# Optimization experiments

Hardware: AMD Instinct MI355X
Metric: run time of the kernel (lower is better)

The kernel has to match this reference:

```python
import jax, jax.numpy as jnp
import numpy as np

H = 8          # n_channels
NEIGHBORS = 5


def setup_inputs() -> dict:
    key = jax.random.key(0)
    k1, k2 = jax.random.split(key)
    B, N, C = 8, 1024, 256
    x = jax.random.normal(k1, (B, N, C), dtype=jnp.float32)
    # torch Linear weight: [out_features, in_features] = [2*H*C, C]
    W_qk = jax.random.normal(k2, (2 * H * C, C), dtype=jnp.float32) * (C ** -0.5)
    return {"x": x, "W_qk": W_qk}


def _forward(x, W_qk):
    B, N, C = x.shape
    scale = C ** -0.5
    qk = (x @ W_qk.T).reshape(B, N, 2, H, C).transpose(2, 0, 3, 1, 4)
    q, k = qk[0], qk[1]                              # [B,H,N,C]
    attn = jax.nn.softmax(jnp.einsum('bhnc,bhmc->bhnm', q, k) * scale, axis=-1)

    # clip(): top-k on detached channel-summed attention
    sum_edge = jnp.sum(jax.lax.stop_gradient(attn), axis=1)   # [B,N,N]
    _, index = jax.lax.top_k(sum_edge, NEIGHBORS)             # [B,N,NEIGHBORS]
    # Faithful to source: every mask row gets 1 at the union of ALL rows'
    # top-k indices (inner loop iterates over all rows of `inds`), plus eye(N).
    flat_idx = index.reshape(B, N * NEIGHBORS)                # [B, N*nb]
    col_mask = jnp.zeros((B, N), dtype=attn.dtype).at[
        jnp.arange(B)[:, None], flat_idx].set(1.0)            # [B,N]
    mask = jnp.maximum(jnp.eye(N, dtype=attn.dtype)[None], col_mask[:, None, :])  # [B,N,N]

    new_edge = mask[:, None] * attn                           # [B,H,N,N]

    # norm_edge(): row norm, then col norm, then row @ col^T
    norm_row = new_edge / (jnp.sum(new_edge, axis=-1, keepdims=True) + 1e-16)
    norm_col = norm_row / (jnp.sum(norm_row, axis=-2, keepdims=True) + 1e-16)
    return jnp.einsum('bhnm,bhkm->bhnk', norm_row, norm_col)  # [B,H,N,N]


def reference(x, W_qk):
    return _forward(x, W_qk)
```

## Files before the change

### kernel.cpp

```cpp
#include <hip/hip_runtime.h>
#include <hip/hip_bf16.h>
#include <cstdint>
#include <cstddef>

#define BB 8
#define HH 8
#define NN 1024
#define CC 256
#define OUTCH 4096

typedef __attribute__((ext_vector_type(8))) __bf16 bf16x8;
typedef __attribute__((ext_vector_type(4))) __bf16 bf16x4;
typedef __attribute__((ext_vector_type(4))) float f32x4;

__device__ inline void async16(const void* g, void* l)
{
  __builtin_amdgcn_global_load_lds(
      reinterpret_cast<const __attribute__((address_space(1))) unsigned int*>(
          reinterpret_cast<uintptr_t>(g)),
      reinterpret_cast<__attribute__((address_space(3))) unsigned int*>(
          reinterpret_cast<uintptr_t>(l)),
      16, 0, 0);
}

__device__ inline float waveMax(float v) {
#pragma unroll
  for (int o = 32; o > 0; o >>= 1) v = fmaxf(v, __shfl_xor(v, o, 64));
  return v;
}
__device__ inline float waveSum(float v) {
#pragma unroll
  for (int o = 32; o > 0; o >>= 1) v += __shfl_xor(v, o, 64);
  return v;
}

__global__ __launch_bounds__(256) void split2_kernel(
    const float* __restrict__ x, const float* __restrict__ W,
    __bf16* __restrict__ xh, __bf16* __restrict__ xl,
    __bf16* __restrict__ Wh, __bf16* __restrict__ Wl)
{
  const int NX = BB * NN * CC / 4;
  int i = blockIdx.x * 256 + threadIdx.x;
  const float* in; __bf16* ph; __bf16* pl; int j;
  if (i < NX) { in = x; ph = xh; pl = xl; j = i; }
  else        { in = W; ph = Wh; pl = Wl; j = i - NX; }
  const float4 v = ((const float4*)in)[j];
  bf16x4 h, l;
  h.x = (__bf16)v.x; l.x = (__bf16)(v.x - (float)h.x);
  h.y = (__bf16)v.y; l.y = (__bf16)(v.y - (float)h.y);
  h.z = (__bf16)v.z; l.z = (__bf16)(v.z - (float)h.z);
  h.w = (__bf16)v.w; l.w = (__bf16)(v.w - (float)h.w);
  ((bf16x4*)ph)[j] = h;
  ((bf16x4*)pl)[j] = l;
}

__global__ __launch_bounds__(256) void xw_mfma_kernel(
    const __bf16* __restrict__ Ah, const __bf16* __restrict__ Al,
    const __bf16* __restrict__ Bh, const __bf16* __restrict__ Bl,
    __bf16* __restrict__ Chi, __bf16* __restrict__ Clo)
{
  __shared__ __bf16 AsH[128 * 32], AsL[128 * 32], BsH[128 * 32], BsL[128 * 32];

  const int tid = threadIdx.x, lane = tid & 63, wid = tid >> 6;
  const int wr = wid >> 1, wc = wid & 1;
  const int bM = blockIdx.y * 128, bN = blockIdx.x * 128;

  const int srow = wid * 16 + (lane >> 2);
  const int scol = (lane & 3) * 8;
  const __bf16* gAh = Ah + (size_t)(bM + srow) * CC + scol;
  const __bf16* gAl = Al + (size_t)(bM + srow) * CC + scol;
  const __bf16* gBh = Bh + (size_t)(bN + srow) * CC + scol;
  const __bf16* gBl = Bl + (size_t)(bN + srow) * CC + scol;
  char* lAh = (char*)AsH + wid * 16 * 64;
  char* lAl = (char*)AsL + wid * 16 * 64;
  char* lBh = (char*)BsH + wid * 16 * 64;
  char* lBl = (char*)BsL + wid * 16 * 64;

  f32x4 acc[4][4];
  const f32x4 z = {0.f, 0.f, 0.f, 0.f};
#pragma unroll
  for (int m = 0; m < 4; ++m)
#pragma unroll
    for (int n = 0; n < 4; ++n) acc[m][n] = z;

  for (int k0 = 0; k0 < CC; k0 += 32) {
    async16(gAh + k0, lAh); async16(gAh + k0 + 64 * CC, lAh + 64 * 64);
    async16(gAl + k0, lAl); async16(gAl + k0 + 64 * CC, lAl + 64 * 64);
    async16(gBh + k0, lBh); async16(gBh + k0 + 64 * CC, lBh + 64 * 64);
    async16(gBl + k0, lBl); async16(gBl + k0 + 64 * CC, lBl + 64 * 64);
    __syncthreads();

    bf16x8 ah[4], al[4], bh_[4], bl_[4];
    const int fb = (lane & 15) * 64 + (lane >> 4) * 16;
#pragma unroll
    for (int m = 0; m < 4; ++m) {
      ah[m] = *(const bf16x8*)((const char*)AsH + (wr * 64 + m * 16) * 64 + fb);
      al[m] = *(const bf16x8*)((const char*)AsL + (wr * 64 + m * 16) * 64 + fb);
    }
#pragma unroll
    for (int n = 0; n < 4; ++n) {
      bh_[n] = *(const bf16x8*)((const char*)BsH + (wc * 64 + n * 16) * 64 + fb);
      bl_[n] = *(const bf16x8*)((const char*)BsL + (wc * 64 + n * 16) * 64 + fb);
    }
#pragma unroll
    for (int m = 0; m < 4; ++m)
#pragma unroll
      for (int n = 0; n < 4; ++n) {
        acc[m][n] = __builtin_amdgcn_mfma_f32_16x16x32_bf16(al[m], bh_[n], acc[m][n], 0, 0, 0);
        acc[m][n] = __builtin_amdgcn_mfma_f32_16x16x32_bf16(ah[m], bl_[n], acc[m][n], 0, 0, 0);
        acc[m][n] = __builtin_amdgcn_mfma_f32_16x16x32_bf16(ah[m], bh_[n], acc[m][n], 0, 0, 0);
      }
    __syncthreads();
  }

  const int fr = lane & 15;
  const int fq = lane >> 4;
#pragma unroll
  for (int m = 0; m < 4; ++m) {
    const int row0 = bM + wr * 64 + m * 16 + fq * 4;
#pragma unroll
    for (int n = 0; n < 4; ++n) {
      const int col = bN + wc * 64 + n * 16 + fr;
#pragma unroll
      for (int r = 0; r < 4; ++r) {
        const float v = acc[m][n][r];
        const __bf16 h = (__bf16)v;
        const __bf16 l = (__bf16)(v - (float)h);
        Chi[(size_t)(row0 + r) * OUTCH + col] = h;
        Clo[(size_t)(row0 + r) * OUTCH + col] = l;
      }
    }
  }
}

__global__ __launch_bounds__(256) void qkt_mfma_kernel(
    const __bf16* __restrict__ Qh, const __bf16* __restrict__ Ql,
    float* __restrict__ outall)
{
  const int f = blockIdx.x;
  const int xcd = f & 7;
  const int g = f >> 3;
  const int bh = xcd + 8 * (g >> 6);
  const int tile = g & 63;
  const int b = bh >> 3, h = bh & 7;
  const size_t qoff = (size_t)b * NN * OUTCH + (size_t)h * CC;
  const size_t koff = qoff + 2048;
  float* C = outall + ((size_t)bh << 20);

  __shared__ __bf16 AsH[128 * 32], AsL[128 * 32], BsH[128 * 32], BsL[128 * 32];

  const int tid = threadIdx.x, lane = tid & 63, wid = tid >> 6;
  const int wr = wid >> 1, wc = wid & 1;
  const int bM = (tile >> 3) * 128, bN = (tile & 7) * 128;

  const int srow = wid * 16 + (lane >> 2);
  const int scol = (lane & 3) * 8;
  const __bf16* gAh = Qh + qoff + (size_t)(bM + srow) * OUTCH + scol;
  const __bf16* gAl = Ql + qoff + (size_t)(bM + srow) * OUTCH + scol;
  const __bf16* gBh = Qh + koff + (size_t)(bN + srow) * OUTCH + scol;
  const __bf16* gBl = Ql + koff + (size_t)(bN + srow) * OUTCH + scol;
  char* lAh = (char*)AsH + wid * 16 * 64;
  char* lAl = (char*)AsL + wid * 16 * 64;
  char* lBh = (char*)BsH + wid * 16 * 64;
  char* lBl = (char*)BsL + wid * 16 * 64;

  f32x4 acc[4][4];
  const f32x4 z = {0.f, 0.f, 0.f, 0.f};
#pragma unroll
  for (int m = 0; m < 4; ++m)
#pragma unroll
    for (int n = 0; n < 4; ++n) acc[m][n] = z;

  for (int k0 = 0; k0 < CC; k0 += 32) {
    async16(gAh + k0, lAh); async16(gAh + k0 + (size_t)64 * OUTCH, lAh + 64 * 64);
    async16(gAl + k0, lAl); async16(gAl + k0 + (size_t)64 * OUTCH, lAl + 64 * 64);
    async16(gBh + k0, lBh); async16(gBh + k0 + (size_t)64 * OUTCH, lBh + 64 * 64);
    async16(gBl + k0, lBl); async16(gBl + k0 + (size_t)64 * OUTCH, lBl + 64 * 64);
    __syncthreads();

    bf16x8 ah[4], al[4], bh_[4], bl_[4];
    const int fb = (lane & 15) * 64 + (lane >> 4) * 16;
#pragma unroll
    for (int m = 0; m < 4; ++m) {
      ah[m] = *(const bf16x8*)((const char*)AsH + (wr * 64 + m * 16) * 64 + fb);
      al[m] = *(const bf16x8*)((const char*)AsL + (wr * 64 + m * 16) * 64 + fb);
    }
#pragma unroll
    for (int n = 0; n < 4; ++n) {
      bh_[n] = *(const bf16x8*)((const char*)BsH + (wc * 64 + n * 16) * 64 + fb);
      bl_[n] = *(const bf16x8*)((const char*)BsL + (wc * 64 + n * 16) * 64 + fb);
    }
#pragma unroll
    for (int m = 0; m < 4; ++m)
#pragma unroll
      for (int n = 0; n < 4; ++n) {
        acc[m][n] = __builtin_amdgcn_mfma_f32_16x16x32_bf16(al[m], bh_[n], acc[m][n], 0, 0, 0);
        acc[m][n] = __builtin_amdgcn_mfma_f32_16x16x32_bf16(ah[m], bl_[n], acc[m][n], 0, 0, 0);
        acc[m][n] = __builtin_amdgcn_mfma_f32_16x16x32_bf16(ah[m], bh_[n], acc[m][n], 0, 0, 0);
      }
    __syncthreads();
  }

  const int fr = lane & 15;
  const int fq = lane >> 4;
#pragma unroll
  for (int m = 0; m < 4; ++m) {
    const int row0 = bM + wr * 64 + m * 16 + fq * 4;
#pragma unroll
    for (int n = 0; n < 4; ++n) {
      const int col = bN + wc * 64 + n * 16 + fr;
#pragma unroll
      for (int r = 0; r < 4; ++r)
        C[(size_t)(row0 + r) * NN + col] = acc[m][n][r] * 0.0625f;
    }
  }
}

__global__ __launch_bounds__(256) void softmax_se_kernel(const float* __restrict__ logits,
                                                         __bf16* __restrict__ attnb,
                                                         float* __restrict__ se)
{
  const int bn = blockIdx.x;
  const int b = bn >> 10;
  const int n = bn & 1023;
  const int t = threadIdx.x;
  const int lane = t & 63, wv = t >> 6;
  __shared__ float wred[4];
  float4 acc = make_float4(0.f, 0.f, 0.f, 0.f);

#pragma unroll 1
  for (int h = 0; h < HH; ++h) {
    const size_t rowbase = (((size_t)(b * HH + h) << 10) + n) << 10;
    const float* ar = logits + rowbase;
    __bf16* arb = attnb + rowbase;
    float4 x = *(const float4*)(ar + (t << 2));
    float mx = waveMax(fmaxf(fmaxf(x.x, x.y), fmaxf(x.z, x.w)));
    if (lane == 0) wred[wv] = mx;
    __syncthreads();
    const float M = fmaxf(fmaxf(wred[0], wred[1]), fmaxf(wred[2], wred[3]));
    __syncthreads();

    float e0 = expf(x.x - M), e1 = expf(x.y - M), e2 = expf(x.z - M), e3 = expf(x.w - M);
    float s = waveSum(e0 + e1 + e2 + e3);
    if (lane == 0) wred[wv] = s;
    __syncthreads();
    const float inv = 1.0f / (wred[0] + wred[1] + wred[2] + wred[3]);

    const float o0 = e0 * inv, o1 = e1 * inv, o2 = e2 * inv, o3 = e3 * inv;
    bf16x4 ob; ob.x = (__bf16)o0; ob.y = (__bf16)o1; ob.z = (__bf16)o2; ob.w = (__bf16)o3;
    *(bf16x4*)(arb + (t << 2)) = ob;
    acc.x += o0; acc.y += o1; acc.z += o2; acc.w += o3;
    __syncthreads();
  }
  *(float4*)(se + (size_t)bn * NN + (t << 2)) = acc;
}

__global__ __launch_bounds__(256) void topk_kernel(const float* __restrict__ se,
                                                   float* __restrict__ colmask)
{
  const int bn = blockIdx.x;
  const int b = bn >> 10;
  const int t = threadIdx.x;
  __shared__ float vals[NN];
  __shared__ unsigned long long red[256];
  const float* rowp = se + (size_t)bn * NN;
  for (int i = t; i < NN; i += 256) vals[i] = rowp[i];
  __syncthreads();

  for (int it = 0; it < 5; ++it) {
    unsigned long long best = 0ull;
    for (int i = t; i < NN; i += 256) {
      const float v = vals[i];
      if (v >= 0.f) {
        unsigned long long key =
            ((unsigned long long)__float_as_uint(v) << 32) | (unsigned)(NN - 1 - i);
        if (key > best) best = key;
      }
    }
    red[t] = best; __syncthreads();
    for (int s = 128; s > 0; s >>= 1) {
      if (t < s) red[t] = red[t] > red[t+s] ? red[t] : red[t+s];
      __syncthreads();
    }
    if (t == 0) {
      const int idx = NN - 1 - (int)(red[0] & 0xFFFFFFFFull);
      colmask[b * NN + idx] = 1.0f;
      vals[idx] = -1.0f;
    }
    __syncthreads();
  }
}

__global__ __launch_bounds__(256) void cs_rs_kernel(const __bf16* __restrict__ attnb,
                                                    const float* __restrict__ colmask,
                                                    float* __restrict__ inv_rs,
                                                    float* __restrict__ part)
{
  const int bh = blockIdx.y;
  const int b = bh >> 3;
  const int chunk = blockIdx.x;
  const int t = threadIdx.x, lane = t & 63, wv = t >> 6;
  const __bf16* ab = attnb + ((size_t)bh << 20);
  const float* cm = colmask + b * NN;
  const int c0 = lane * 16;

  float cmv[16];
#pragma unroll
  for (int q = 0; q < 4; ++q) {
    const float4 c4 = *(const float4*)(cm + c0 + q * 4);
    cmv[q*4+0] = c4.x; cmv[q*4+1] = c4.y; cmv[q*4+2] = c4.z; cmv[q*4+3] = c4.w;
  }

  float a[16];
#pragma unroll
  for (int j = 0; j < 16; ++j) a[j] = 0.f;

  const int nbase = chunk * 64 + wv * 16;
#pragma unroll 1
  for (int r = 0; r < 16; ++r) {
    const int n = nbase + r;
    const __bf16* rowp = ab + ((size_t)n << 10) + c0;
    const bf16x8 v0 = *(const bf16x8*)(rowp);
    const bf16x8 v1 = *(const bf16x8*)(rowp + 8);
    float e[16];
    float rsum = 0.f;
#pragma unroll
    for (int j = 0; j < 8; ++j) {
      const float val = ((cmv[j] != 0.f) || (c0 + j == n)) ? (float)v0[j] : 0.f;
      e[j] = val; rsum += val;
    }
#pragma unroll
    for (int j = 0; j < 8; ++j) {
      const float val = ((cmv[8+j] != 0.f) || (c0 + 8 + j == n)) ? (float)v1[j] : 0.f;
      e[8+j] = val; rsum += val;
    }
    rsum = waveSum(rsum);
    const float ir = 1.0f / (rsum + 1e-16f);
    if (lane == 0) inv_rs[bh * NN + n] = ir;
#pragma unroll
    for (int j = 0; j < 16; ++j) a[j] += e[j] * ir;
  }

  __shared__ float l[4][NN];
#pragma unroll
  for (int j = 0; j < 16; ++j) l[wv][c0 + j] = a[j];
  __syncthreads();
  const int m0 = t << 2;
  float4 o;
  o.x = l[0][m0+0] + l[1][m0+0] + l[2][m0+0] + l[3][m0+0];
  o.y = l[0][m0+1] + l[1][m0+1] + l[2][m0+1] + l[3][m0+1];
  o.z = l[0][m0+2] + l[1][m0+2] + l[2][m0+2] + l[3][m0+2];
  o.w = l[0][m0+3] + l[1][m0+3] + l[2][m0+3] + l[3][m0+3];
  *(float4*)(part + (((size_t)chunk * (BB*HH) + bh) << 10) + m0) = o;
}

__global__ __launch_bounds__(256) void cs_fin_kernel(const float* __restrict__ part,
                                                     float* __restrict__ isc)
{
  const int bh = blockIdx.x;
  const int m0 = threadIdx.x << 2;
  float a0 = 0.f, a1 = 0.f, a2 = 0.f, a3 = 0.f;
#pragma unroll
  for (int c = 0; c < 16; ++c) {
    const float4 p = *(const float4*)(part + (((size_t)c * (BB*HH) + bh) << 10) + m0);
    a0 += p.x; a1 += p.y; a2 += p.z; a3 += p.w;
  }
  float4 o;
  o.x = 1.0f / sqrtf(a0 + 1e-16f);
  o.y = 1.0f / sqrtf(a1 + 1e-16f);
  o.z = 1.0f / sqrtf(a2 + 1e-16f);
  o.w = 1.0f / sqrtf(a3 + 1e-16f);
  *(float4*)(isc + ((size_t)bh << 10) + m0) = o;
}

__global__ __launch_bounds__(256) void g_kernel(const __bf16* __restrict__ attnb,
                                                const float* __restrict__ colmask,
                                                const float* __restrict__ inv_rs,
                                                const float* __restrict__ isc,
                                                __bf16* __restrict__ Gb)
{
  const size_t idx = ((size_t)blockIdx.x * 256 + threadIdx.x) << 2;
  const size_t row = idx >> 10;
  const int m = (int)(idx & 1023);
  const int n = (int)(row & 1023);
  const int bh = (int)(row >> 10);
  const int b = bh >> 3;
  const bf16x4 vb = *(const bf16x4*)(attnb + idx);
  const float4 c = *(const float4*)(colmask + b * NN + m);
  const float4 s = *(const float4*)(isc + ((size_t)bh << 10) + m);
  const float ir = inv_rs[row];
  bf16x4 o;
  o.x = (__bf16)((((c.x != 0.f) || (m + 0 == n)) ? (float)vb.x : 0.f) * ir * s.x);
  o.y = (__bf16)((((c.y != 0.f) || (m + 1 == n)) ? (float)vb.y : 0.f) * ir * s.y);
  o.z = (__bf16)((((c.z != 0.f) || (m + 2 == n)) ? (float)vb.z : 0.f) * ir * s.z);
  o.w = (__bf16)((((c.w != 0.f) || (m + 3 == n)) ? (float)vb.w : 0.f) * ir * s.w);
  *(bf16x4*)(Gb + idx) = o;
}

__global__ __launch_bounds__(256) void ggt_mfma_kernel(const __bf16* __restrict__ Gball,
                                                       float* __restrict__ outall)
{
  const int f = blockIdx.x;
  const int xcd = f & 7;
  const int g = f >> 3;
  const int bh = xcd + 8 * (g / 36);
  int tt = g % 36;

  const __bf16* A = Gball + ((size_t)bh << 20);
  float* C = outall + ((size_t)bh << 20);

  int ti = 0;
#pragma unroll
  for (int r = 0; r < 8; ++r) {
    const int len = 8 - r;
    if (tt < len) { ti = r; break; }
    tt -= len;
  }
  const int tj = ti + tt;

  __shared__ __bf16 As[2][128 * 32];
  __shared__ __bf16 Bs[2][128 * 32];

  const int tid  = threadIdx.x;
  const int lane = tid & 63;
  const int wid  = tid >> 6;
  const int wr   = wid >> 1;
  const int wc   = wid & 1;
  const int bM   = ti * 128;
  const int bN   = tj * 128;

  const int srow = wid * 16 + (lane >> 2);
  const int scol = (lane & 3) * 8;
  const __bf16* gA = A + (size_t)(bM + srow) * NN + scol;
  const __bf16* gB = A + (size_t)(bN + srow) * NN + scol;
  const int lofs = wid * 16 * 64;

  f32x4 acc[4][4];
  const f32x4 z = {0.f, 0.f, 0.f, 0.f};
#pragma unroll
  for (int m = 0; m < 4; ++m)
#pragma unroll
    for (int n = 0; n < 4; ++n) acc[m][n] = z;

  const int fb = (lane & 15) * 64 + (lane >> 4) * 16;

  async16(gA,           (char*)As[0] + lofs);
  async16(gA + 64 * NN, (char*)As[0] + lofs + 64 * 64);
  async16(gB,           (char*)Bs[0] + lofs);
  async16(gB + 64 * NN, (char*)Bs[0] + lofs + 64 * 64);

  int cur = 0;
#pragma unroll 1
  for (int k0 = 0; k0 < NN - 32; k0 += 32) {
    const int nxt = cur ^ 1;
    async16(gA + k0 + 32,           (char*)As[nxt] + lofs);
    async16(gA + k0 + 32 + 64 * NN, (char*)As[nxt] + lofs + 64 * 64);
    async16(gB + k0 + 32,           (char*)Bs[nxt] + lofs);
    async16(gB + k0 + 32 + 64 * NN, (char*)Bs[nxt] + lofs + 64 * 64);
    asm volatile("s_waitcnt vmcnt(4)" ::: "memory");
    __builtin_amdgcn_s_barrier();
    __builtin_amdgcn_sched_barrier(0);

    bf16x8 a[4], b[4];
#pragma unroll
    for (int m = 0; m < 4; ++m)
      a[m] = *(const bf16x8*)((const char*)As[cur] + (wr * 64 + m * 16) * 64 + fb);
#pragma unroll
    for (int n = 0; n < 4; ++n)
      b[n] = *(const bf16x8*)((const char*)Bs[cur] + (wc * 64 + n * 16) * 64 + fb);
#pragma unroll
    for (int m = 0; m < 4; ++m)
#pragma unroll
      for (int n = 0; n < 4; ++n)
        acc[m][n] = __builtin_amdgcn_mfma_f32_16x16x32_bf16(a[m], b[n], acc[m][n], 0, 0, 0);
    __builtin_amdgcn_s_barrier();
    __builtin_amdgcn_sched_barrier(0);
    cur ^= 1;
  }

  asm volatile("s_waitcnt vmcnt(0)" ::: "memory");
  __builtin_amdgcn_s_barrier();
  __builtin_amdgcn_sched_barrier(0);
  {
    bf16x8 a[4], b[4];
#pragma unroll
    for (int m = 0; m < 4; ++m)
      a[m] = *(const bf16x8*)((const char*)As[cur] + (wr * 64 + m * 16) * 64 + fb);
#pragma unroll
    for (int n = 0; n < 4; ++n)
      b[n] = *(const bf16x8*)((const char*)Bs[cur] + (wc * 64 + n * 16) * 64 + fb);
#pragma unroll
    for (int m = 0; m < 4; ++m)
#pragma unroll
      for (int n = 0; n < 4; ++n)
        acc[m][n] = __builtin_amdgcn_mfma_f32_16x16x32_bf16(a[m], b[n], acc[m][n], 0, 0, 0);
  }

  const int fr = lane & 15;
  const int fq = lane >> 4;
#pragma unroll
  for (int m = 0; m < 4; ++m) {
    const int row0 = bM + wr * 64 + m * 16 + fq * 4;
#pragma unroll
    for (int n = 0; n < 4; ++n) {
      const int col = bN + wc * 64 + n * 16 + fr;
#pragma unroll
      for (int r = 0; r < 4; ++r)
        C[(size_t)(row0 + r) * NN + col] = acc[m][n][r];
    }
  }
  if (ti != tj) {
#pragma unroll
    for (int m = 0; m < 4; ++m) {
      const int colT = bM + wr * 64 + m * 16 + fq * 4;
#pragma unroll
      for (int n = 0; n < 4; ++n) {
        const int rowT = bN + wc * 64 + n * 16 + fr;
        *(f32x4*)(C + (size_t)rowT * NN + colT) = acc[m][n];
      }
    }
  }
}

extern "C" void kernel_launch(void* const* d_in, const int* in_sizes, int n_in,
                              void* d_out, int out_size, void* d_ws, size_t ws_size,
                              hipStream_t stream)
{
  const float* x = (const float*)d_in[0];
  const float* W = (const float*)d_in[1];
  float* logits = (float*)d_out;
  char* ws = (char*)d_ws;

  __bf16* qk_hi = (__bf16*)(ws + ((size_t)0   << 20));
  __bf16* qk_lo = (__bf16*)(ws + ((size_t)64  << 20));
  __bf16* attnb = (__bf16*)(ws + ((size_t)0   << 20));
  __bf16* x_hi  = (__bf16*)(ws + ((size_t)128 << 20));
  __bf16* x_lo  = (__bf16*)(ws + ((size_t)132 << 20));
  __bf16* W_hi  = (__bf16*)(ws + ((size_t)136 << 20));
  __bf16* W_lo  = (__bf16*)(ws + ((size_t)138 << 20));
  float*  se    = (float*)(ws + ((size_t)144 << 20));
  float*  cmask = (float*)(ws + ((size_t)176 << 20));
  float*  irs   = (float*)(ws + ((size_t)177 << 20));
  float*  isc   = (float*)(ws + ((size_t)178 << 20));
  float*  csp   = (float*)(ws + ((size_t)180 << 20));
  __bf16* Gb    = (__bf16*)(ws + ((size_t)192 << 20));

  hipLaunchKernelGGL(split2_kernel, dim3((BB*NN*CC + OUTCH*CC) / 4 / 256), dim3(256), 0, stream,
                     x, W, x_hi, x_lo, W_hi, W_lo);

  hipLaunchKernelGGL(xw_mfma_kernel, dim3(OUTCH/128, (BB*NN)/128, 1), dim3(256), 0, stream,
                     x_hi, x_lo, W_hi, W_lo, qk_hi, qk_lo);

  hipLaunchKernelGGL(qkt_mfma_kernel, dim3(64 * 64), dim3(256), 0, stream,
                     qk_hi, qk_lo, logits);

  hipLaunchKernelGGL(softmax_se_kernel, dim3(BB*NN), dim3(256), 0, stream,
                     logits, attnb, se);

  hipMemsetAsync(cmask, 0, (size_t)BB * NN * 4, stream);
  hipLaunchKernelGGL(topk_kernel, dim3(BB*NN), dim3(256), 0, stream, se, cmask);

  hipLaunchKernelGGL(cs_rs_kernel, dim3(16, BB*HH), dim3(256), 0, stream,
                     attnb, cmask, irs, csp);
  hipLaunchKernelGGL(cs_fin_kernel, dim3(BB*HH), dim3(256), 0, stream, csp, isc);

  hipLaunchKernelGGL(g_kernel, dim3((BB*HH*NN*(long long)NN) / 4 / 256), dim3(256), 0, stream,
                     attnb, cmask, irs, isc, Gb);

  hipLaunchKernelGGL(ggt_mfma_kernel, dim3(36 * 64), dim3(256), 0, stream,
                     Gb, logits);

  (void)in_sizes; (void)n_in; (void)out_size; (void)ws_size;
}
```

Before: 553.0 us.

## Fold Wq·Wk^T into per-head projection to halve XW GEMM output

Rewrites q·k^T as x·(Wq_h^T Wk_h)·x^T: a small per-head 256x256 matrix P_h is precomputed from transposed W slices, then y = x·P_h (2048 output channels instead of 4096), and the logits GEMM multiplies y against x directly. This halves the large projection GEMM's FLOPs and output bytes, and the qk^T stage now reads x as the B operand. The trade is extra small kernels (transpose-split of W, per-head P GEMM) and an extra rounding step through the hi/lo bf16 split of P, which may shift numerics slightly.

Result: faster. 522.6 us (-5.5%).

```diff
diff --git a/kernel.cpp b/kernel.cpp
--- a/kernel.cpp
+++ b/kernel.cpp
@@ -7,7 +7,7 @@
 #define HH 8
 #define NN 1024
 #define CC 256
-#define OUTCH 4096
+#define YC 2048
 
 typedef __attribute__((ext_vector_type(8))) __bf16 bf16x8;
 typedef __attribute__((ext_vector_type(4))) __bf16 bf16x4;
@@ -34,31 +34,57 @@
   return v;
 }
 
-__global__ __launch_bounds__(256) void split2_kernel(
-    const float* __restrict__ x, const float* __restrict__ W,
-    __bf16* __restrict__ xh, __bf16* __restrict__ xl,
-    __bf16* __restrict__ Wh, __bf16* __restrict__ Wl)
-{
-  const int NX = BB * NN * CC / 4;
-  int i = blockIdx.x * 256 + threadIdx.x;
-  const float* in; __bf16* ph; __bf16* pl; int j;
-  if (i < NX) { in = x; ph = xh; pl = xl; j = i; }
-  else        { in = W; ph = Wh; pl = Wl; j = i - NX; }
-  const float4 v = ((const float4*)in)[j];
+__global__ __launch_bounds__(256) void split_kernel(const float* __restrict__ in,
+                                                    __bf16* __restrict__ hi,
+                                                    __bf16* __restrict__ lo)
+{
+  const int i = blockIdx.x * 256 + threadIdx.x;
+  const float4 v = ((const float4*)in)[i];
   bf16x4 h, l;
   h.x = (__bf16)v.x; l.x = (__bf16)(v.x - (float)h.x);
   h.y = (__bf16)v.y; l.y = (__bf16)(v.y - (float)h.y);
   h.z = (__bf16)v.z; l.z = (__bf16)(v.z - (float)h.z);
   h.w = (__bf16)v.w; l.w = (__bf16)(v.w - (float)h.w);
-  ((bf16x4*)ph)[j] = h;
-  ((bf16x4*)pl)[j] = l;
-}
-
-__global__ __launch_bounds__(256) void xw_mfma_kernel(
-    const __bf16* __restrict__ Ah, const __bf16* __restrict__ Al,
-    const __bf16* __restrict__ Bh, const __bf16* __restrict__ Bl,
-    __bf16* __restrict__ Chi, __bf16* __restrict__ Clo)
-{
+  ((bf16x4*)hi)[i] = h;
+  ((bf16x4*)lo)[i] = l;
+}
+
+__global__ __launch_bounds__(256) void wt_split_kernel(const float* __restrict__ W,
+                                                       __bf16* __restrict__ Th,
+                                                       __bf16* __restrict__ Tl)
+{
+  const int z = blockIdx.z;
+  const float* Wb = W + ((size_t)z << 16);
+  __shared__ float t[64][65];
+  const int i0 = blockIdx.x * 64, c0 = blockIdx.y * 64;
+  const int tr = threadIdx.x >> 6;
+  const int tc = threadIdx.x & 63;
+#pragma unroll
+  for (int rr = 0; rr < 64; rr += 4)
+    t[rr + tr][tc] = Wb[(size_t)(i0 + rr + tr) * 256 + c0 + tc];
+  __syncthreads();
+  __bf16* Thb = Th + ((size_t)z << 16);
+  __bf16* Tlb = Tl + ((size_t)z << 16);
+#pragma unroll
+  for (int cc = 0; cc < 64; cc += 4) {
+    const int c = cc + tr, i = tc;
+    const float v = t[i][c];
+    const __bf16 h = (__bf16)v;
+    Thb[(size_t)(c0 + c) * 256 + i0 + i] = h;
+    Tlb[(size_t)(c0 + c) * 256 + i0 + i] = (__bf16)(v - (float)h);
+  }
+}
+
+__global__ __launch_bounds__(256) void pp_mfma_kernel(
+    const __bf16* __restrict__ Th, const __bf16* __restrict__ Tl,
+    __bf16* __restrict__ Phi, __bf16* __restrict__ Plo)
+{
+  const int h = blockIdx.z;
+  const __bf16* Ah = Th + ((size_t)(8 + h) << 16);
+  const __bf16* Al = Tl + ((size_t)(8 + h) << 16);
+  const __bf16* Bh = Th + ((size_t)h << 16);
+  const __bf16* Bl = Tl + ((size_t)h << 16);
+
   __shared__ __bf16 AsH[128 * 32], AsL[128 * 32], BsH[128 * 32], BsL[128 * 32];
 
   const int tid = threadIdx.x, lane = tid & 63, wid = tid >> 6;
@@ -77,11 +103,11 @@
   char* lBl = (char*)BsL + wid * 16 * 64;
 
   f32x4 acc[4][4];
-  const f32x4 z = {0.f, 0.f, 0.f, 0.f};
+  const f32x4 z4 = {0.f, 0.f, 0.f, 0.f};
 #pragma unroll
   for (int m = 0; m < 4; ++m)
 #pragma unroll
-    for (int n = 0; n < 4; ++n) acc[m][n] = z;
+    for (int n = 0; n < 4; ++n) acc[m][n] = z4;
 
   for (int k0 = 0; k0 < CC; k0 += 32) {
     async16(gAh + k0, lAh); async16(gAh + k0 + 64 * CC, lAh + 64 * 64);
@@ -117,6 +143,84 @@
   const int fq = lane >> 4;
 #pragma unroll
   for (int m = 0; m < 4; ++m) {
+    const int row0 = h * 256 + bM + wr * 64 + m * 16 + fq * 4;
+#pragma unroll
+    for (int n = 0; n < 4; ++n) {
+      const int col = bN + wc * 64 + n * 16 + fr;
+#pragma unroll
+      for (int r = 0; r < 4; ++r) {
+        const float v = acc[m][n][r];
+        const __bf16 hh = (__bf16)v;
+        Phi[(size_t)(row0 + r) * CC + col] = hh;
+        Plo[(size_t)(row0 + r) * CC + col] = (__bf16)(v - (float)hh);
+      }
+    }
+  }
+}
+
+__global__ __launch_bounds__(256) void y_mfma_kernel(
+    const __bf16* __restrict__ Ah, const __bf16* __restrict__ Al,
+    const __bf16* __restrict__ Bh, const __bf16* __restrict__ Bl,
+    __bf16* __restrict__ Chi, __bf16* __restrict__ Clo)
+{
+  __shared__ __bf16 AsH[128 * 32], AsL[128 * 32], BsH[128 * 32], BsL[128 * 32];
+
+  const int tid = threadIdx.x, lane = tid & 63, wid = tid >> 6;
+  const int wr = wid >> 1, wc = wid & 1;
+  const int bM = blockIdx.y * 128, bN = blockIdx.x * 128;
+
+  const int srow = wid * 16 + (lane >> 2);
+  const int scol = (lane & 3) * 8;
+  const __bf16* gAh = Ah + (size_t)(bM + srow) * CC + scol;
+  const __bf16* gAl = Al + (size_t)(bM + srow) * CC + scol;
+  const __bf16* gBh = Bh + (size_t)(bN + srow) * CC + scol;
+  const __bf16* gBl = Bl + (size_t)(bN + srow) * CC + scol;
+  char* lAh = (char*)AsH + wid * 16 * 64;
+  char* lAl = (char*)AsL + wid * 16 * 64;
+  char* lBh = (char*)BsH + wid * 16 * 64;
+  char* lBl = (char*)BsL + wid * 16 * 64;
+
+  f32x4 acc[4][4];
+  const f32x4 z = {0.f, 0.f, 0.f, 0.f};
+#pragma unroll
+  for (int m = 0; m < 4; ++m)
+#pragma unroll
+    for (int n = 0; n < 4; ++n) acc[m][n] = z;
+
+  for (int k0 = 0; k0 < CC; k0 += 32) {
+    async16(gAh + k0, lAh); async16(gAh + k0 + 64 * CC, lAh + 64 * 64);
+    async16(gAl + k0, lAl); async16(gAl + k0 + 64 * CC, lAl + 64 * 64);
+    async16(gBh + k0, lBh); async16(gBh + k0 + 64 * CC, lBh + 64 * 64);
+    async16(gBl + k0, lBl); async16(gBl + k0 + 64 * CC, lBl + 64 * 64);
+    __syncthreads();
+
+    bf16x8 ah[4], al[4], bh_[4], bl_[4];
+    const int fb = (lane & 15) * 64 + (lane >> 4) * 16;
+#pragma unroll
+    for (int m = 0; m < 4; ++m) {
+      ah[m] = *(const bf16x8*)((const char*)AsH + (wr * 64 + m * 16) * 64 + fb);
+      al[m] = *(const bf16x8*)((const char*)AsL + (wr * 64 + m * 16) * 64 + fb);
+    }
+#pragma unroll
+    for (int n = 0; n < 4; ++n) {
+      bh_[n] = *(const bf16x8*)((const char*)BsH + (wc * 64 + n * 16) * 64 + fb);
+      bl_[n] = *(const bf16x8*)((const char*)BsL + (wc * 64 + n * 16) * 64 + fb);
+    }
+#pragma unroll
+    for (int m = 0; m < 4; ++m)
+#pragma unroll
+      for (int n = 0; n < 4; ++n) {
+        acc[m][n] = __builtin_amdgcn_mfma_f32_16x16x32_bf16(al[m], bh_[n], acc[m][n], 0, 0, 0);
+        acc[m][n] = __builtin_amdgcn_mfma_f32_16x16x32_bf16(ah[m], bl_[n], acc[m][n], 0, 0, 0);
+        acc[m][n] = __builtin_amdgcn_mfma_f32_16x16x32_bf16(ah[m], bh_[n], acc[m][n], 0, 0, 0);
+      }
+    __syncthreads();
+  }
+
+  const int fr = lane & 15;
+  const int fq = lane >> 4;
+#pragma unroll
+  for (int m = 0; m < 4; ++m) {
     const int row0 = bM + wr * 64 + m * 16 + fq * 4;
 #pragma unroll
     for (int n = 0; n < 4; ++n) {
@@ -125,16 +229,16 @@
       for (int r = 0; r < 4; ++r) {
         const float v = acc[m][n][r];
         const __bf16 h = (__bf16)v;
-        const __bf16 l = (__bf16)(v - (float)h);
-        Chi[(size_t)(row0 + r) * OUTCH + col] = h;
-        Clo[(size_t)(row0 + r) * OUTCH + col] = l;
+        Chi[(size_t)(row0 + r) * YC + col] = h;
+        Clo[(size_t)(row0 + r) * YC + col] = (__bf16)(v - (float)h);
       }
     }
   }
 }
 
 __global__ __launch_bounds__(256) void qkt_mfma_kernel(
-    const __bf16* __restrict__ Qh, const __bf16* __restrict__ Ql,
+    const __bf16* __restrict__ Yh, const __bf16* __restrict__ Yl,
+    const __bf16* __restrict__ Xh, const __bf16* __restrict__ Xl,
     float* __restrict__ outall)
 {
   const int f = blockIdx.x;
@@ -143,8 +247,8 @@
   const int bh = xcd + 8 * (g >> 6);
   const int tile = g & 63;
   const int b = bh >> 3, h = bh & 7;
-  const size_t qoff = (size_t)b * NN * OUTCH + (size_t)h * CC;
-  const size_t koff = qoff + 2048;
+  const size_t aoff = (size_t)b * NN * YC + (size_t)h * CC;
+  const size_t boff = (size_t)b * NN * CC;
   float* C = outall + ((size_t)bh << 20);
 
   __shared__ __bf16 AsH[128 * 32], AsL[128 * 32], BsH[128 * 32], BsL[128 * 32];
@@ -155,10 +259,10 @@
 
   const int srow = wid * 16 + (lane >> 2);
   const int scol = (lane & 3) * 8;
-  const __bf16* gAh = Qh + qoff + (size_t)(bM + srow) * OUTCH + scol;
-  const __bf16* gAl = Ql + qoff + (size_t)(bM + srow) * OUTCH + scol;
-  const __bf16* gBh = Qh + koff + (size_t)(bN + srow) * OUTCH + scol;
-  const __bf16* gBl = Ql + koff + (size_t)(bN + srow) * OUTCH + scol;
+  const __bf16* gAh = Yh + aoff + (size_t)(bM + srow) * YC + scol;
+  const __bf16* gAl = Yl + aoff + (size_t)(bM + srow) * YC + scol;
+  const __bf16* gBh = Xh + boff + (size_t)(bN + srow) * CC + scol;
+  const __bf16* gBl = Xl + boff + (size_t)(bN + srow) * CC + scol;
   char* lAh = (char*)AsH + wid * 16 * 64;
   char* lAl = (char*)AsL + wid * 16 * 64;
   char* lBh = (char*)BsH + wid * 16 * 64;
@@ -172,10 +276,10 @@
     for (int n = 0; n < 4; ++n) acc[m][n] = z;
 
   for (int k0 = 0; k0 < CC; k0 += 32) {
-    async16(gAh + k0, lAh); async16(gAh + k0 + (size_t)64 * OUTCH, lAh + 64 * 64);
-    async16(gAl + k0, lAl); async16(gAl + k0 + (size_t)64 * OUTCH, lAl + 64 * 64);
-    async16(gBh + k0, lBh); async16(gBh + k0 + (size_t)64 * OUTCH, lBh + 64 * 64);
-    async16(gBl + k0, lBl); async16(gBl + k0 + (size_t)64 * OUTCH, lBl + 64 * 64);
+    async16(gAh + k0, lAh); async16(gAh + k0 + (size_t)64 * YC, lAh + 64 * 64);
+    async16(gAl + k0, lAl); async16(gAl + k0 + (size_t)64 * YC, lAl + 64 * 64);
+    async16(gBh + k0, lBh); async16(gBh + k0 + (size_t)64 * CC, lBh + 64 * 64);
+    async16(gBl + k0, lBl); async16(gBl + k0 + (size_t)64 * CC, lBl + 64 * 64);
     __syncthreads();
 
     bf16x8 ah[4], al[4], bh_[4], bl_[4];
@@ -531,13 +635,15 @@
   float* logits = (float*)d_out;
   char* ws = (char*)d_ws;
 
-  __bf16* qk_hi = (__bf16*)(ws + ((size_t)0   << 20));
-  __bf16* qk_lo = (__bf16*)(ws + ((size_t)64  << 20));
+  __bf16* y_hi  = (__bf16*)(ws + ((size_t)0   << 20));
+  __bf16* y_lo  = (__bf16*)(ws + ((size_t)32  << 20));
   __bf16* attnb = (__bf16*)(ws + ((size_t)0   << 20));
   __bf16* x_hi  = (__bf16*)(ws + ((size_t)128 << 20));
   __bf16* x_lo  = (__bf16*)(ws + ((size_t)132 << 20));
-  __bf16* W_hi  = (__bf16*)(ws + ((size_t)136 << 20));
-  __bf16* W_lo  = (__bf16*)(ws + ((size_t)138 << 20));
+  __bf16* T_hi  = (__bf16*)(ws + ((size_t)136 << 20));
+  __bf16* T_lo  = (__bf16*)(ws + ((size_t)138 << 20));
+  __bf16* P_hi  = (__bf16*)(ws + ((size_t)140 << 20));
+  __bf16* P_lo  = (__bf16*)(ws + ((size_t)142 << 20));
   float*  se    = (float*)(ws + ((size_t)144 << 20));
   float*  cmask = (float*)(ws + ((size_t)176 << 20));
   float*  irs   = (float*)(ws + ((size_t)177 << 20));
@@ -545,14 +651,18 @@
   float*  csp   = (float*)(ws + ((size_t)180 << 20));
   __bf16* Gb    = (__bf16*)(ws + ((size_t)192 << 20));
 
-  hipLaunchKernelGGL(split2_kernel, dim3((BB*NN*CC + OUTCH*CC) / 4 / 256), dim3(256), 0, stream,
-                     x, W, x_hi, x_lo, W_hi, W_lo);
-
-  hipLaunchKernelGGL(xw_mfma_kernel, dim3(OUTCH/128, (BB*NN)/128, 1), dim3(256), 0, stream,
-                     x_hi, x_lo, W_hi, W_lo, qk_hi, qk_lo);
+  hipLaunchKernelGGL(split_kernel, dim3(BB*NN*CC/4/256), dim3(256), 0, stream,
+                     x, x_hi, x_lo);
+  hipLaunchKernelGGL(wt_split_kernel, dim3(4, 4, 16), dim3(256), 0, stream,
+                     W, T_hi, T_lo);
+  hipLaunchKernelGGL(pp_mfma_kernel, dim3(2, 2, 8), dim3(256), 0, stream,
+                     T_hi, T_lo, P_hi, P_lo);
+
+  hipLaunchKernelGGL(y_mfma_kernel, dim3(YC/128, (BB*NN)/128, 1), dim3(256), 0, stream,
+                     x_hi, x_lo, P_hi, P_lo, y_hi, y_lo);
 
   hipLaunchKernelGGL(qkt_mfma_kernel, dim3(64 * 64), dim3(256), 0, stream,
-                     qk_hi, qk_lo, logits);
+                     y_hi, y_lo, x_hi, x_lo, logits);
 
   hipLaunchKernelGGL(softmax_se_kernel, dim3(BB*NN), dim3(256), 0, stream,
                      logits, attnb, se);
```
